# Kernel tuning notes

Hardware: AMD Instinct MI355X
Metric: run time of the kernel (lower is better)

The kernel has to match this reference:

```python
import jax, jax.numpy as jnp
import numpy as np

EMB = 32  # DGM_c.input_dim

def setup_inputs() -> dict:
    key = jax.random.key(0)
    k1, k2, k3 = jax.random.split(key, 3)
    G, n, F = 32, 1024, 128
    N = G * n
    x = jax.random.normal(k1, (N, F), dtype=jnp.float32)
    W = jax.random.normal(k2, (F, EMB), dtype=jnp.float32) / np.sqrt(F)
    temperature = jnp.float32(1.0)   # nn.Parameter init 1.0
    threshold = jnp.float32(0.5)     # nn.Parameter init 0.5
    batch = jnp.repeat(jnp.arange(G, dtype=jnp.int32), n)  # equal-sized graphs
    edge_index = jax.random.randint(k3, (2, 262144), 0, N, dtype=jnp.int32)
    return {"x": x, "W": W, "temperature": temperature, "threshold": threshold,
            "batch": batch, "edge_index": edge_index, "num_graphs": G}


def reference(x, W, temperature, threshold, batch, edge_index, num_graphs):
    # x: [N, F]; equal-sized graphs of n nodes each (batch is sorted, contiguous)
    N = x.shape[0]
    G = num_graphs
    n = N // G

    # embed_f: linear projection to EMB dims (edge structure unused by this embed_f)
    xe = x @ W                                  # [N, EMB]

    # scale<0 branch fires only for the FIRST graph; centroid/scale are detached
    x0 = xe[:n]                                 # graph 0 embedding
    centroid = jax.lax.stop_gradient(jnp.mean(x0, axis=0))             # [EMB]
    scale = jax.lax.stop_gradient(0.9 / jnp.max(jnp.abs(x0 - centroid)))

    xg = ((xe - centroid) * scale).reshape(G, n, EMB)

    # squared pairwise euclidean distances per graph (cdist**2, clamped >= 0)
    sq = jnp.sum(xg * xg, axis=-1)              # [G, n]
    D = jnp.maximum(sq[:, :, None] + sq[:, None, :]
                    - 2.0 * jnp.einsum('gnd,gmd->gnm', xg, xg), 0.0)   # [G, n, n]

    A = jax.nn.sigmoid(temperature * (jnp.abs(threshold) - D))         # [G, n, n]

    # sigmoid > 0 everywhere => dense_to_sparse keeps every entry, row-major,
    # with per-graph node offsets added back.
    edge_weight = A.reshape(-1)                 # [G*n*n]
    ii = jnp.arange(n, dtype=jnp.int32)
    gi = jnp.broadcast_to(ii[:, None], (n, n)).reshape(-1)  # row index
    gj = jnp.broadcast_to(ii[None, :], (n, n)).reshape(-1)  # col index
    off = (jnp.arange(G, dtype=jnp.int32) * n)[:, None]     # [G, 1]
    src = (off + gi[None, :]).reshape(-1)
    dst = (off + gj[None, :]).reshape(-1)
    edge_index_out = jnp.stack([src, dst])      # [2, G*n*n]

    return xe, edge_index_out, edge_weight
```

## Files before the change

### kernel.cpp

```cpp
#include <hip/hip_runtime.h>

#define FDIM 128
#define EMB 32

__global__ __launch_bounds__(256) void k_gemm(const float* __restrict__ x,
                                              const float* __restrict__ Wm,
                                              float* __restrict__ xe) {
    __shared__ float sW[FDIM * EMB];
    const int t = threadIdx.x;
#pragma unroll
    for (int i = 0; i < (FDIM * EMB) / (256 * 4); ++i) {
        int idx = (t + i * 256) * 4;
        *(float4*)(sW + idx) = *(const float4*)(Wm + idx);
    }
    __syncthreads();

    const int r0 = blockIdx.x * 128 + (t >> 3) * 4;
    const int e0 = (t & 7) * 4;

    float acc[4][4];
#pragma unroll
    for (int i = 0; i < 4; ++i)
#pragma unroll
        for (int j = 0; j < 4; ++j) acc[i][j] = 0.f;

    for (int k = 0; k < FDIM; k += 4) {
        float4 w0 = *(const float4*)(sW + (k + 0) * EMB + e0);
        float4 w1 = *(const float4*)(sW + (k + 1) * EMB + e0);
        float4 w2 = *(const float4*)(sW + (k + 2) * EMB + e0);
        float4 w3 = *(const float4*)(sW + (k + 3) * EMB + e0);
#pragma unroll
        for (int rr = 0; rr < 4; ++rr) {
            float4 xq = *(const float4*)(x + (size_t)(r0 + rr) * FDIM + k);
            acc[rr][0] += xq.x * w0.x + xq.y * w1.x + xq.z * w2.x + xq.w * w3.x;
            acc[rr][1] += xq.x * w0.y + xq.y * w1.y + xq.z * w2.y + xq.w * w3.y;
            acc[rr][2] += xq.x * w0.z + xq.y * w1.z + xq.z * w2.z + xq.w * w3.z;
            acc[rr][3] += xq.x * w0.w + xq.y * w1.w + xq.z * w2.w + xq.w * w3.w;
        }
    }

#pragma unroll
    for (int rr = 0; rr < 4; ++rr) {
        const size_t r = (size_t)(r0 + rr);
        float4 o; o.x = acc[rr][0]; o.y = acc[rr][1]; o.z = acc[rr][2]; o.w = acc[rr][3];
        *(float4*)(xe + r * EMB + e0) = o;
    }
}

__global__ __launch_bounds__(256) void k_stats_a(const float* __restrict__ xe,
                                                 float* __restrict__ psum,
                                                 float* __restrict__ pmin,
                                                 float* __restrict__ pmax) {
    __shared__ float rs[256], rmn[256], rmx[256];
    const int t = threadIdx.x;
    const int d = t & 31, rg = t >> 5;
    const int r0 = blockIdx.x * 32;

    float s = 0.f, mn = 3.4e38f, mx = -3.4e38f;
#pragma unroll
    for (int it = 0; it < 4; ++it) {
        float v = xe[(size_t)(r0 + rg + it * 8) * EMB + d];
        s += v;
        mn = fminf(mn, v);
        mx = fmaxf(mx, v);
    }
    rs[t] = s; rmn[t] = mn; rmx[t] = mx;
    __syncthreads();
#pragma unroll
    for (int st = 128; st >= 32; st >>= 1) {
        if (t < st) {
            rs[t] += rs[t + st];
            rmn[t] = fminf(rmn[t], rmn[t + st]);
            rmx[t] = fmaxf(rmx[t], rmx[t + st]);
        }
        __syncthreads();
    }
    if (t < 32) {
        psum[blockIdx.x * 32 + t] = rs[t];
        pmin[blockIdx.x * 32 + t] = rmn[t];
        pmax[blockIdx.x * 32 + t] = rmx[t];
    }
}

__global__ __launch_bounds__(64) void k_stats_b(const float* __restrict__ psum,
                                                const float* __restrict__ pmin,
                                                const float* __restrict__ pmax,
                                                int nb, int n,
                                                float* __restrict__ stats) {
    const int t = threadIdx.x;
    const int d = t & 31;
    float s = 0.f, mn = 3.4e38f, mx = -3.4e38f;
    for (int b = 0; b < nb; ++b) {
        s += psum[b * 32 + d];
        mn = fminf(mn, pmin[b * 32 + d]);
        mx = fmaxf(mx, pmax[b * 32 + d]);
    }
    const float c = s / (float)n;
    float dev = fmaxf(mx - c, c - mn);
#pragma unroll
    for (int off = 16; off >= 1; off >>= 1)
        dev = fmaxf(dev, __shfl_xor(dev, off, 32));
    if (t < 32) stats[t] = c;
    if (t == 0) stats[EMB] = 0.9f / dev;
}

#define LDST 36
__global__ __launch_bounds__(256) void k_edges(const float* __restrict__ xe,
                                               const float* __restrict__ stats,
                                               const float* __restrict__ tptr,
                                               const float* __restrict__ thptr,
                                               float* __restrict__ wts,
                                               float* __restrict__ srcp,
                                               float* __restrict__ dstp,
                                               int n) {
    __shared__ float shA[64 * LDST];
    __shared__ float shB[64 * LDST];
    __shared__ float sqA[64], sqB[64];

    const int g = blockIdx.z;
    const int i0 = blockIdx.y * 64, j0 = blockIdx.x * 64;
    const int t = threadIdx.x;
    const float scale = stats[EMB];

    const float* baseA = xe + ((size_t)g * n + i0) * EMB;
    const float* baseB = xe + ((size_t)g * n + j0) * EMB;

#pragma unroll
    for (int c = 0; c < 2; ++c) {
        int id = t + c * 256;
        int row = id >> 3;
        int dc = (id & 7) * 4;
        float4 cen = *(const float4*)(stats + dc);
        float4 va = *(const float4*)(baseA + (size_t)row * EMB + dc);
        float4 vb = *(const float4*)(baseB + (size_t)row * EMB + dc);
        va.x = (va.x - cen.x) * scale; va.y = (va.y - cen.y) * scale;
        va.z = (va.z - cen.z) * scale; va.w = (va.w - cen.w) * scale;
        vb.x = (vb.x - cen.x) * scale; vb.y = (vb.y - cen.y) * scale;
        vb.z = (vb.z - cen.z) * scale; vb.w = (vb.w - cen.w) * scale;
        *(float4*)(shA + row * LDST + dc) = va;
        *(float4*)(shB + row * LDST + dc) = vb;
    }
    __syncthreads();

    if (t < 64) {
        float s = 0.f;
#pragma unroll
        for (int d = 0; d < EMB; d += 4) {
            float4 v = *(const float4*)(shA + t * LDST + d);
            s += v.x * v.x + v.y * v.y + v.z * v.z + v.w * v.w;
        }
        sqA[t] = s;
    } else if (t < 128) {
        int r = t - 64;
        float s = 0.f;
#pragma unroll
        for (int d = 0; d < EMB; d += 4) {
            float4 v = *(const float4*)(shB + r * LDST + d);
            s += v.x * v.x + v.y * v.y + v.z * v.z + v.w * v.w;
        }
        sqB[r] = s;
    }
    __syncthreads();

    const int ti = t >> 4, tj = t & 15;
    float acc[4][4];
#pragma unroll
    for (int i = 0; i < 4; ++i)
#pragma unroll
        for (int j = 0; j < 4; ++j) acc[i][j] = 0.f;

    for (int d = 0; d < EMB; d += 4) {
        float4 a[4], b[4];
#pragma unroll
        for (int u = 0; u < 4; ++u)
            a[u] = *(const float4*)(shA + (ti * 4 + u) * LDST + d);
#pragma unroll
        for (int v = 0; v < 4; ++v)
            b[v] = *(const float4*)(shB + (v * 16 + tj) * LDST + d);
#pragma unroll
        for (int u = 0; u < 4; ++u)
#pragma unroll
            for (int v = 0; v < 4; ++v)
                acc[u][v] += a[u].x * b[v].x + a[u].y * b[v].y +
                             a[u].z * b[v].z + a[u].w * b[v].w;
    }

    const float T = *tptr;
    const float TH = fabsf(*thptr);
    const int gn = g * n;
    const size_t gbase = (size_t)g * n * n;

    float dval[4];
#pragma unroll
    for (int v = 0; v < 4; ++v) dval[v] = (float)(gn + j0 + v * 16 + tj);

#pragma unroll
    for (int u = 0; u < 4; ++u) {
        const int row = i0 + ti * 4 + u;
        const float sa = sqA[ti * 4 + u];
        const float sv = (float)(gn + row);
        const size_t rbase = gbase + (size_t)row * n;
#pragma unroll
        for (int v = 0; v < 4; ++v) {
            const int col = j0 + v * 16 + tj;
            float D = fmaxf(sa + sqB[v * 16 + tj] - 2.f * acc[u][v], 0.f);
            float z = T * (TH - D);
            float Av = __builtin_amdgcn_rcpf(1.f + __expf(-z));
            wts[rbase + col]  = Av;
            srcp[rbase + col] = sv;
            dstp[rbase + col] = dval[v];
        }
    }
}

extern "C" void kernel_launch(void* const* d_in, const int* in_sizes, int n_in,
                              void* d_out, int out_size, void* d_ws, size_t ws_size,
                              hipStream_t stream) {
    const float* x     = (const float*)d_in[0];
    const float* Wm    = (const float*)d_in[1];
    const float* tptr  = (const float*)d_in[2];
    const float* thptr = (const float*)d_in[3];

    const int N = in_sizes[0] / FDIM;
    const long long rem = (long long)out_size - (long long)N * EMB;
    int G = (rem > 0) ? (int)((3LL * N * N) / rem) : 32;
    if (G <= 0) G = 32;
    const int n = N / G;
    const int nb = n / 32;

    float* out  = (float*)d_out;
    float* xe   = out;
    const long long M = (long long)G * n * n;
    float* srcp = out + (size_t)N * EMB;
    float* dstp = srcp + (size_t)M;
    float* wts  = dstp + (size_t)M;

    float* stats = (float*)d_ws;
    float* psum  = stats + 64;
    float* pmin  = psum + (size_t)nb * 32;
    float* pmax  = pmin + (size_t)nb * 32;

    k_gemm<<<N / 128, 256, 0, stream>>>(x, Wm, xe);
    k_stats_a<<<nb, 256, 0, stream>>>(xe, psum, pmin, pmax);
    k_stats_b<<<1, 64, 0, stream>>>(psum, pmin, pmax, nb, n, stats);
    dim3 ge(n / 64, n / 64, G);
    k_edges<<<ge, 256, 0, stream>>>(xe, stats, tptr, thptr, wts, srcp, dstp, n);
}
```

Baseline: 112.0 us.

## Remap column ownership for float4 output stores and swizzle shared B tile

Each thread now owns four adjacent columns (tj*4+v) instead of strided ones (v*16+tj), so the weight, src and dst outputs can be written with 128-bit float4 stores rather than scalar stores. Since this makes the B-row reads in shared memory stride by four rows, the B tile is stored with an XOR swizzle on the column offset to avoid LDS bank conflicts, and the sqB and GEMM reads apply the same swizzle. The kernel is dominated by writing the large output, so wider stores are meant to cut store-instruction count and improve coalescing. The risk is that each wavefront store instruction now spans a wider, less contiguous address range per row.

```diff
diff --git a/kernel.cpp b/kernel.cpp
--- a/kernel.cpp
+++ b/kernel.cpp
@@ -130,6 +130,7 @@
         int id = t + c * 256;
         int row = id >> 3;
         int dc = (id & 7) * 4;
+        int dswz = dc ^ (((row >> 2) & 7) << 2);
         float4 cen = *(const float4*)(stats + dc);
         float4 va = *(const float4*)(baseA + (size_t)row * EMB + dc);
         float4 vb = *(const float4*)(baseB + (size_t)row * EMB + dc);
@@ -138,7 +139,7 @@
         vb.x = (vb.x - cen.x) * scale; vb.y = (vb.y - cen.y) * scale;
         vb.z = (vb.z - cen.z) * scale; vb.w = (vb.w - cen.w) * scale;
         *(float4*)(shA + row * LDST + dc) = va;
-        *(float4*)(shB + row * LDST + dc) = vb;
+        *(float4*)(shB + row * LDST + dswz) = vb;
     }
     __syncthreads();
 
@@ -152,10 +153,11 @@
         sqA[t] = s;
     } else if (t < 128) {
         int r = t - 64;
+        int key = ((r >> 2) & 7) << 2;
         float s = 0.f;
 #pragma unroll
         for (int d = 0; d < EMB; d += 4) {
-            float4 v = *(const float4*)(shB + r * LDST + d);
+            float4 v = *(const float4*)(shB + r * LDST + (d ^ key));
             s += v.x * v.x + v.y * v.y + v.z * v.z + v.w * v.w;
         }
         sqB[r] = s;
@@ -163,6 +165,7 @@
     __syncthreads();
 
     const int ti = t >> 4, tj = t & 15;
+    const int bkey = (tj & 7) << 2;
     float acc[4][4];
 #pragma unroll
     for (int i = 0; i < 4; ++i)
@@ -174,9 +177,10 @@
 #pragma unroll
         for (int u = 0; u < 4; ++u)
             a[u] = *(const float4*)(shA + (ti * 4 + u) * LDST + d);
+        const int dsw = d ^ bkey;
 #pragma unroll
         for (int v = 0; v < 4; ++v)
-            b[v] = *(const float4*)(shB + (v * 16 + tj) * LDST + d);
+            b[v] = *(const float4*)(shB + (tj * 4 + v) * LDST + dsw);
 #pragma unroll
         for (int u = 0; u < 4; ++u)
 #pragma unroll
@@ -190,26 +194,33 @@
     const int gn = g * n;
     const size_t gbase = (size_t)g * n * n;
 
-    float dval[4];
-#pragma unroll
-    for (int v = 0; v < 4; ++v) dval[v] = (float)(gn + j0 + v * 16 + tj);
+    const float4 sq4 = *(const float4*)(sqB + tj * 4);
+    const float dbase = (float)(gn + j0 + tj * 4);
+    float4 dst4; dst4.x = dbase; dst4.y = dbase + 1.f; dst4.z = dbase + 2.f; dst4.w = dbase + 3.f;
 
 #pragma unroll
     for (int u = 0; u < 4; ++u) {
         const int row = i0 + ti * 4 + u;
         const float sa = sqA[ti * 4 + u];
+        const size_t off = gbase + (size_t)row * n + j0 + tj * 4;
+
+        float4 w;
+        {
+            float D0 = fmaxf(sa + sq4.x - 2.f * acc[u][0], 0.f);
+            float D1 = fmaxf(sa + sq4.y - 2.f * acc[u][1], 0.f);
+            float D2 = fmaxf(sa + sq4.z - 2.f * acc[u][2], 0.f);
+            float D3 = fmaxf(sa + sq4.w - 2.f * acc[u][3], 0.f);
+            w.x = __builtin_amdgcn_rcpf(1.f + __expf(-(T * (TH - D0))));
+            w.y = __builtin_amdgcn_rcpf(1.f + __expf(-(T * (TH - D1))));
+            w.z = __builtin_amdgcn_rcpf(1.f + __expf(-(T * (TH - D2))));
+            w.w = __builtin_amdgcn_rcpf(1.f + __expf(-(T * (TH - D3))));
+        }
+        *(float4*)(wts + off) = w;
+
         const float sv = (float)(gn + row);
-        const size_t rbase = gbase + (size_t)row * n;
-#pragma unroll
-        for (int v = 0; v < 4; ++v) {
-            const int col = j0 + v * 16 + tj;
-            float D = fmaxf(sa + sqB[v * 16 + tj] - 2.f * acc[u][v], 0.f);
-            float z = T * (TH - D);
-            float Av = __builtin_amdgcn_rcpf(1.f + __expf(-z));
-            wts[rbase + col]  = Av;
-            srcp[rbase + col] = sv;
-            dstp[rbase + col] = dval[v];
-        }
+        float4 s4; s4.x = sv; s4.y = sv; s4.z = sv; s4.w = sv;
+        *(float4*)(srcp + off) = s4;
+        *(float4*)(dstp + off) = dst4;
     }
 }
 
```

Result: no change. 110.7 us (-1.2%).
